# Kernel optimization log

Hardware: AMD Instinct MI355X
Metric: run time of the kernel (lower is better)

Reference implementation:

```python
import jax, jax.numpy as jnp
import numpy as np

N_NODES = 100000


def _gcn_layer(x, src, dst, W, b, n):
    # PyG GCNConv: x' = x @ W, then symmetric-normalized aggregation with
    # self-loops (fill value 1), then + bias.
    h = x @ W  # [n, out]
    loop = jnp.arange(n, dtype=src.dtype)
    s = jnp.concatenate([src, loop])  # sources incl. self-loops
    d = jnp.concatenate([dst, loop])  # destinations incl. self-loops
    # degree computed on destination (col) with unit edge weights
    deg = jax.ops.segment_sum(jnp.ones_like(d, dtype=h.dtype), d, num_segments=n)
    dinv = jnp.where(deg > 0, jax.lax.rsqrt(deg), 0.0)
    norm = dinv[s] * dinv[d]  # [E+n]
    msg = h[s] * norm[:, None]  # gather + scale, [E+n, out]
    out = jax.ops.segment_sum(msg, d, num_segments=n)  # scatter-add
    return out + b


def setup_inputs() -> dict:
    key = jax.random.key(0)
    k1, k2, k3, k4, k5, k6 = jax.random.split(key, 6)
    in_c, hid_c, out_c = 5, 128, 64
    E = 1600000
    x = jax.random.normal(k1, (N_NODES, in_c), dtype=jnp.float32)
    edge_index = jax.random.randint(k2, (2, E), 0, N_NODES, dtype=jnp.int64)
    # Glorot-style init like PyG's Linear
    W1 = jax.random.normal(k3, (in_c, hid_c), dtype=jnp.float32) / np.sqrt(in_c)
    b1 = jnp.zeros((hid_c,), dtype=jnp.float32)
    W2 = jax.random.normal(k4, (hid_c, out_c), dtype=jnp.float32) / np.sqrt(hid_c)
    b2 = jnp.zeros((out_c,), dtype=jnp.float32)
    return {"x": x, "edge_index": edge_index, "W1": W1, "b1": b1, "W2": W2, "b2": b2}


def reference(x, edge_index, W1, b1, W2, b2):
    src, dst = edge_index[0], edge_index[1]
    n = x.shape[0]
    h = _gcn_layer(x, src, dst, W1, b1, n)
    h = jax.nn.relu(h)
    out = _gcn_layer(h, src, dst, W2, b2, n)
    return out
```

## Files before the change

kernel.cpp:

```cpp
#include <hip/hip_runtime.h>
#include <hip/hip_fp16.h>

#define IN_C 5
#define HID  128
#define OUTC 64

#define NBUCK_MAX 512
#define BCAP      4800
#define BIN_GRID  512
#define BIN_PER   3328
#define BIN_ITERS 13

typedef _Float16 f16x8 __attribute__((ext_vector_type(8)));
typedef float    f32x4 __attribute__((ext_vector_type(4)));

__global__ void __launch_bounds__(256)
k_init(const float* __restrict__ W2, __half* __restrict__ W2p,
       int* __restrict__ bucket_cnt) {
    if (blockIdx.x < 2) bucket_cnt[blockIdx.x * 256 + threadIdx.x] = 0;
    int i = blockIdx.x * 256 + threadIdx.x;
    int j = i & 7;
    int lane = (i >> 3) & 63;
    int kk = (i >> 9) & 3;
    int nt = i >> 11;
    int k = kk * 32 + (lane >> 4) * 8 + j;
    int nn = nt * 16 + (lane & 15);
    W2p[i] = __float2half(W2[k * OUTC + nn]);
}

__global__ void __launch_bounds__(256)
k_bin(const int* __restrict__ src, const int* __restrict__ dst,
      int* __restrict__ bucket_cnt, unsigned* __restrict__ binned, int E) {
    __shared__ int hist[NBUCK_MAX], base[NBUCK_MAX], lstart[NBUCK_MAX], cur[NBUCK_MAX];
    __shared__ unsigned staged[BIN_PER];
    __shared__ unsigned short sbuck[BIN_PER];
    int t = threadIdx.x;
    hist[t] = 0; hist[t + 256] = 0;
    __syncthreads();
    int per = (E + gridDim.x - 1) / gridDim.x;
    int lo = blockIdx.x * per, hi = min(E, lo + per);
    int ds[BIN_ITERS], ss[BIN_ITERS];
#pragma unroll
    for (int i = 0; i < BIN_ITERS; ++i) {
        int e = lo + t + i * 256;
        if (e < hi) {
            int d = dst[e];
            ds[i] = d; ss[i] = src[e];
            atomicAdd(&hist[d >> 8], 1);
        } else ds[i] = -1;
    }
    __syncthreads();
    if (hist[t] > 0)       base[t] = atomicAdd(&bucket_cnt[t], hist[t]);
    if (hist[t + 256] > 0) base[t + 256] = atomicAdd(&bucket_cnt[t + 256], hist[t + 256]);
    lstart[t] = hist[t]; lstart[t + 256] = hist[t + 256];
    __syncthreads();
#pragma unroll
    for (int off = 1; off < NBUCK_MAX; off <<= 1) {
        int a0 = (t >= off) ? lstart[t - off] : 0;
        int a1 = (t + 256 >= off) ? lstart[t + 256 - off] : 0;
        __syncthreads();
        lstart[t] += a0; lstart[t + 256] += a1;
        __syncthreads();
    }
    {
        int e0 = lstart[t] - hist[t];
        int e1 = lstart[t + 256] - hist[t + 256];
        __syncthreads();
        lstart[t] = e0; lstart[t + 256] = e1;
        cur[t] = e0; cur[t + 256] = e1;
    }
    __syncthreads();
#pragma unroll
    for (int i = 0; i < BIN_ITERS; ++i) {
        if (ds[i] >= 0) {
            int d = ds[i];
            int b = d >> 8;
            int pos = atomicAdd(&cur[b], 1);
            staged[pos] = ((unsigned)ss[i] << 8) | (unsigned)(d & 255);
            sbuck[pos] = (unsigned short)b;
        }
    }
    __syncthreads();
    int mtot = hi - lo;
    for (int s = t; s < mtot; s += 256) {
        int b = sbuck[s];
        binned[(size_t)b * BCAP + base[b] + (s - lstart[b])] = staged[s];
    }
}

__global__ void __launch_bounds__(256)
k_csr(const unsigned* __restrict__ binned, const int* __restrict__ bucket_cnt,
      const float* __restrict__ x,
      int* __restrict__ rowptr, int* __restrict__ cnt, float* __restrict__ dinv,
      __half* __restrict__ xs, int* __restrict__ col, int n, int nb) {
    __shared__ int sc[NBUCK_MAX];
    __shared__ int hist[256], sc2[256], cur[256];
    __shared__ int staged[BCAP];
    int b = blockIdx.x;
    int t = threadIdx.x;

    sc[t]       = (t < nb) ? bucket_cnt[t] : 0;
    sc[t + 256] = (t + 256 < nb) ? bucket_cnt[t + 256] : 0;
    __syncthreads();
#pragma unroll
    for (int off = 1; off < NBUCK_MAX; off <<= 1) {
        int a0 = (t >= off) ? sc[t - off] : 0;
        int a1 = (t + 256 >= off) ? sc[t + 256 - off] : 0;
        __syncthreads();
        sc[t] += a0; sc[t + 256] += a1;
        __syncthreads();
    }
    int m = bucket_cnt[b];
    int ebase = (b == 0) ? 0 : sc[b - 1];
    const unsigned* bin = binned + (size_t)b * BCAP;

    hist[t] = 0;
    __syncthreads();
    for (int e = t; e < m; e += 256)
        atomicAdd(&hist[bin[e] & 255], 1);
    __syncthreads();

    int h = hist[t];
    sc2[t] = h;
    __syncthreads();
#pragma unroll
    for (int off = 1; off < 256; off <<= 1) {
        int a = (t >= off) ? sc2[t - off] : 0;
        __syncthreads();
        sc2[t] += a;
        __syncthreads();
    }
    int rs = sc2[t] - h;
    cur[t] = rs;

    int v = b * 256 + t;
    if (v < n) {
        rowptr[v] = ebase + rs;
        cnt[v] = h;
        float dv = rsqrtf(1.0f + (float)h);
        dinv[v] = dv;
        const float* xp = x + (size_t)v * IN_C;
        __half2 hh[4];
        hh[0] = __floats2half2_rn(xp[0] * dv, xp[1] * dv);
        hh[1] = __floats2half2_rn(xp[2] * dv, xp[3] * dv);
        hh[2] = __floats2half2_rn(xp[4] * dv, 0.f);
        hh[3] = __floats2half2_rn(0.f, 0.f);
        *(uint4*)(xs + (size_t)v * 8) = *(uint4*)hh;
    }
    __syncthreads();
    for (int e = t; e < m; e += 256) {
        unsigned p = bin[e];
        int pos = atomicAdd(&cur[p & 255], 1);
        staged[pos] = (int)(p >> 8);
    }
    __syncthreads();
    for (int e = t; e < m; e += 256)
        col[ebase + e] = staged[e];
}

#define NB 64
#define H1STRIDE 132
__global__ void __launch_bounds__(256, 7)
k_fused(const __half* __restrict__ xs, const float* __restrict__ dinv,
        const int* __restrict__ rowptr, const int* __restrict__ cnt,
        const int* __restrict__ col,
        const float* __restrict__ W1, const float* __restrict__ b1,
        const __half* __restrict__ W2p, __half* __restrict__ g2, int n) {
    __shared__ __half sh_h1[NB * H1STRIDE];
    __shared__ float sh_xa[NB * 9];
    __shared__ float sh_dinv[NB];
    __shared__ int sh_start[NB], sh_len[NB];
    __shared__ __half2 sh_w1[IN_C * 64];
    __shared__ float sh_b1[HID];
    int t = threadIdx.x;
    int base = blockIdx.x * NB;

    for (int idx = t; idx < IN_C * 64; idx += 256) {
        int k = idx >> 6, jp = idx & 63;
        float2 w = *(const float2*)(W1 + k * HID + 2 * jp);
        sh_w1[idx] = __floats2half2_rn(w.x, w.y);
    }
    if (t < HID) sh_b1[t] = b1[t];

    if (t < NB) {
        int v = base + t;
        if (v < n) {
            sh_start[t] = rowptr[v];
            sh_len[t]   = cnt[v];
            sh_dinv[t]  = dinv[v];
        } else {
            sh_start[t] = 0; sh_len[t] = 0; sh_dinv[t] = 0.f;
        }
    }
    __syncthreads();

    {
        int q = t & 7;
#pragma unroll
        for (int half = 0; half < 2; ++half) {
            int vl = (t >> 3) + half * 32;
            int v = base + vl;
            int start = sh_start[vl], len = sh_len[vl];
            float a0 = 0.f, a1 = 0.f, a2 = 0.f, a3 = 0.f, a4 = 0.f;
            if (q == 0 && v < n) {
                uint4 r = *(const uint4*)(xs + (size_t)v * 8);
                const __half2* h = (const __half2*)&r;
                float2 f0 = __half22float2(h[0]), f1 = __half22float2(h[1]), f2 = __half22float2(h[2]);
                a0 = f0.x; a1 = f0.y; a2 = f1.x; a3 = f1.y; a4 = f2.x;
            }
            for (int k = q; k < len; k += 8) {
                int s = col[start + k];
                uint4 r = *(const uint4*)(xs + (size_t)s * 8);
                const __half2* h = (const __half2*)&r;
                float2 f0 = __half22float2(h[0]), f1 = __half22float2(h[1]), f2 = __half22float2(h[2]);
                a0 += f0.x; a1 += f0.y; a2 += f1.x; a3 += f1.y; a4 += f2.x;
            }
#pragma unroll
            for (int d = 1; d <= 4; d <<= 1) {
                a0 += __shfl_down(a0, d, 64);
                a1 += __shfl_down(a1, d, 64);
                a2 += __shfl_down(a2, d, 64);
                a3 += __shfl_down(a3, d, 64);
                a4 += __shfl_down(a4, d, 64);
            }
            if (q == 0) {
                float* sx = sh_xa + vl * 9;
                sx[0] = a0; sx[1] = a1; sx[2] = a2; sx[3] = a3; sx[4] = a4;
            }
        }
    }
    __syncthreads();

    {
        int v = t >> 2;
        const float* xa = sh_xa + v * 9;
        float x0 = xa[0], x1 = xa[1], x2 = xa[2], x3 = xa[3], x4 = xa[4];
        float dv = sh_dinv[v];
        __half* hrow = sh_h1 + v * H1STRIDE;
#pragma unroll
        for (int i = 0; i < 16; ++i) {
            int jp = (t & 3) + 4 * i;
            float2 w0 = __half22float2(sh_w1[jp]);
            float2 w1v = __half22float2(sh_w1[64 + jp]);
            float2 w2v = __half22float2(sh_w1[128 + jp]);
            float2 w3 = __half22float2(sh_w1[192 + jp]);
            float2 w4 = __half22float2(sh_w1[256 + jp]);
            float acc0 = x0 * w0.x + x1 * w1v.x + x2 * w2v.x + x3 * w3.x + x4 * w4.x;
            float acc1 = x0 * w0.y + x1 * w1v.y + x2 * w2v.y + x3 * w3.y + x4 * w4.y;
            int j0 = jp * 2;
            float2 bb = *(const float2*)(sh_b1 + j0);
            *(__half2*)(hrow + j0) =
                __floats2half2_rn(fmaxf(acc0 * dv + bb.x, 0.f), fmaxf(acc1 * dv + bb.y, 0.f));
        }
    }
    __syncthreads();

    {
        int w = t >> 6;
        int lane = t & 63;
        int quad = lane >> 4, nn = lane & 15;
        const __half* arow = sh_h1 + (size_t)(w * 16 + nn) * H1STRIDE + quad * 8;
        f16x8 afr[4];
#pragma unroll
        for (int kk = 0; kk < 4; ++kk)
            afr[kk] = *(const f16x8*)(arow + kk * 32);

        const f16x8* bp = (const f16x8*)W2p + lane;
#pragma unroll
        for (int nt = 0; nt < 4; ++nt) {
            f32x4 acc = {0.f, 0.f, 0.f, 0.f};
#pragma unroll
            for (int kk = 0; kk < 4; ++kk)
                acc = __builtin_amdgcn_mfma_f32_16x16x32_f16(
                    afr[kk], bp[(nt * 4 + kk) * 64], acc, 0, 0, 0);
#pragma unroll
            for (int r = 0; r < 4; ++r) {
                int vl = w * 16 + quad * 4 + r;
                int v = base + vl;
                if (v < n)
                    g2[(size_t)v * OUTC + nt * 16 + nn] =
                        __float2half(acc[r] * sh_dinv[vl]);
            }
        }
    }
}


#define MIX_LO(A, W) \
    asm("v_fma_mix_f32 %0, %1, %2, %0 op_sel:[0,0,0] op_sel_hi:[1,0,0]" \
        : "+v"(A) : "v"(W), "v"(one))
#define MIX_HI(A, W) \
    asm("v_fma_mix_f32 %0, %1, %2, %0 op_sel:[1,0,0] op_sel_hi:[1,0,0]" \
        : "+v"(A) : "v"(W), "v"(one))

#define ACC8(P, R)            \
    do {                      \
        MIX_LO(P##0, (R).x);  \
        MIX_HI(P##1, (R).x);  \
        MIX_LO(P##2, (R).y);  \
        MIX_HI(P##3, (R).y);  \
        MIX_LO(P##4, (R).z);  \
        MIX_HI(P##5, (R).z);  \
        MIX_LO(P##6, (R).w);  \
        MIX_HI(P##7, (R).w);  \
    } while (0)

__global__ void __launch_bounds__(256)
k_agg2(const __half* __restrict__ g2, const float* __restrict__ dinv,
       const int* __restrict__ rowptr, const int* __restrict__ cnt,
       const int* __restrict__ col, const float* __restrict__ b2,
       float* __restrict__ out, int n) {
    int t = threadIdx.x;
    int g = t >> 3;
    int oct = t & 7;
    int v = blockIdx.x * 32 + g;
    if (v >= n) return;

    int start = rowptr[v], len = cnt[v];
    float one = 1.0f;

    float a0 = 0.f, a1 = 0.f, a2 = 0.f, a3 = 0.f,
          a4 = 0.f, a5 = 0.f, a6 = 0.f, a7 = 0.f;
    float c0 = 0.f, c1 = 0.f, c2 = 0.f, c3 = 0.f,
          c4 = 0.f, c5 = 0.f, c6 = 0.f, c7 = 0.f;

    int it = 0;
    for (; it + 2 <= len; it += 2) {
        int s0 = col[start + it];
        int s1 = col[start + it + 1];
        uint4 r0 = *(const uint4*)(g2 + ((size_t)s0 << 6) + (oct << 3));
        uint4 r1 = *(const uint4*)(g2 + ((size_t)s1 << 6) + (oct << 3));
        ACC8(a, r0);
        ACC8(c, r1);
    }
    if (it < len) {
        int s0 = col[start + it];
        uint4 r0 = *(const uint4*)(g2 + ((size_t)s0 << 6) + (oct << 3));
        ACC8(a, r0);
    }

    {
        uint4 rs = *(const uint4*)(g2 + ((size_t)v << 6) + (oct << 3));
        ACC8(a, rs);
    }

    a0 += c0; a1 += c1; a2 += c2; a3 += c3;
    a4 += c4; a5 += c5; a6 += c6; a7 += c7;

    float dv = dinv[v];
    const float* bp = b2 + (oct << 3);
    float4 bb0 = *(const float4*)bp;
    float4 bb1 = *(const float4*)(bp + 4);

    float4 o0 = make_float4(dv * a0 + bb0.x, dv * a1 + bb0.y,
                            dv * a2 + bb0.z, dv * a3 + bb0.w);
    float4 o1 = make_float4(dv * a4 + bb1.x, dv * a5 + bb1.y,
                            dv * a6 + bb1.z, dv * a7 + bb1.w);
    float4* op = (float4*)(out + ((size_t)v << 6) + (oct << 3));
    op[0] = o0;
    op[1] = o1;
}


extern "C" void kernel_launch(void* const* d_in, const int* in_sizes, int n_in,
                              void* d_out, int out_size, void* d_ws, size_t ws_size,
                              hipStream_t stream) {
    const float* x  = (const float*)d_in[0];
    const int*   ei = (const int*)d_in[1];
    const float* W1 = (const float*)d_in[2];
    const float* b1 = (const float*)d_in[3];
    const float* W2 = (const float*)d_in[4];
    const float* b2 = (const float*)d_in[5];
    float*       out = (float*)d_out;

    const int n = in_sizes[0] / IN_C;
    const int E = in_sizes[1] / 2;
    const int* src = ei;
    const int* dst = ei + E;
    const int nbuck = (n + 255) / 256;

    char* ws = (char*)d_ws;
    size_t off = 0;
    int* cnt         = (int*)(ws + off); off += (size_t)n * 4;
    int* rowptr      = (int*)(ws + off); off += (size_t)n * 4;
    int* col         = (int*)(ws + off); off += (size_t)E * 4;
    float* dinv      = (float*)(ws + off); off += (size_t)n * 4;
    __half* xs       = (__half*)(ws + off); off += (size_t)n * 8 * 2;
    __half* g2       = (__half*)(ws + off); off += (size_t)n * OUTC * 2;
    __half* W2p      = (__half*)(ws + off); off += (size_t)HID * OUTC * 2;
    int* bucket_cnt  = (int*)(ws + off); off += NBUCK_MAX * 4;
    unsigned* binned = (unsigned*)(ws + off); off += (size_t)NBUCK_MAX * BCAP * 4;

    const int B = 256;

    k_init<<<(HID * OUTC) / B, B, 0, stream>>>(W2, W2p, bucket_cnt);
    k_bin<<<BIN_GRID, B, 0, stream>>>(src, dst, bucket_cnt, binned, E);
    k_csr<<<nbuck, B, 0, stream>>>(binned, bucket_cnt, x,
                                   rowptr, cnt, dinv, xs, col, n, nbuck);

    k_fused<<<(n + NB - 1) / NB, B, 0, stream>>>(xs, dinv, rowptr, cnt, col,
                                                 W1, b1, W2p, g2, n);
    k_agg2<<<(n + 31) / 32, B, 0, stream>>>(g2, dinv, rowptr, cnt, col, b2, out, n);
}
```

Before: 171.8 us.

## Replace bucketed binning CSR build with global-atomic degree count and scatter

Replaces the two-pass bucket binning (block-local histogram, staged bucket writes, per-bucket LDS counting sort) with a classic CSR build: zero counts, global atomic degree count, block sums, scan, and atomic-cursor scatter of source indices into col. This removes the intermediate binned buffer and its LDS-heavy staging, at the cost of many scattered global atomics and uncoalesced col writes. Edge order within each row becomes nondeterministic, and the build now takes more, smaller kernel launches.

```diff
diff --git a/kernel.cpp b/kernel.cpp
--- a/kernel.cpp
+++ b/kernel.cpp
@@ -6,18 +6,12 @@
 #define OUTC 64
 
 #define NBUCK_MAX 512
-#define BCAP      4800
-#define BIN_GRID  512
-#define BIN_PER   3328
-#define BIN_ITERS 13
 
 typedef _Float16 f16x8 __attribute__((ext_vector_type(8)));
 typedef float    f32x4 __attribute__((ext_vector_type(4)));
 
 __global__ void __launch_bounds__(256)
-k_init(const float* __restrict__ W2, __half* __restrict__ W2p,
-       int* __restrict__ bucket_cnt) {
-    if (blockIdx.x < 2) bucket_cnt[blockIdx.x * 256 + threadIdx.x] = 0;
+k_init(const float* __restrict__ W2, __half* __restrict__ W2p) {
     int i = blockIdx.x * 256 + threadIdx.x;
     int j = i & 7;
     int lane = (i >> 3) & 63;
@@ -28,79 +22,53 @@
     W2p[i] = __float2half(W2[k * OUTC + nn]);
 }
 
-__global__ void __launch_bounds__(256)
-k_bin(const int* __restrict__ src, const int* __restrict__ dst,
-      int* __restrict__ bucket_cnt, unsigned* __restrict__ binned, int E) {
-    __shared__ int hist[NBUCK_MAX], base[NBUCK_MAX], lstart[NBUCK_MAX], cur[NBUCK_MAX];
-    __shared__ unsigned staged[BIN_PER];
-    __shared__ unsigned short sbuck[BIN_PER];
-    int t = threadIdx.x;
-    hist[t] = 0; hist[t + 256] = 0;
-    __syncthreads();
-    int per = (E + gridDim.x - 1) / gridDim.x;
-    int lo = blockIdx.x * per, hi = min(E, lo + per);
-    int ds[BIN_ITERS], ss[BIN_ITERS];
-#pragma unroll
-    for (int i = 0; i < BIN_ITERS; ++i) {
-        int e = lo + t + i * 256;
-        if (e < hi) {
-            int d = dst[e];
-            ds[i] = d; ss[i] = src[e];
-            atomicAdd(&hist[d >> 8], 1);
-        } else ds[i] = -1;
-    }
-    __syncthreads();
-    if (hist[t] > 0)       base[t] = atomicAdd(&bucket_cnt[t], hist[t]);
-    if (hist[t + 256] > 0) base[t + 256] = atomicAdd(&bucket_cnt[t + 256], hist[t + 256]);
-    lstart[t] = hist[t]; lstart[t + 256] = hist[t + 256];
-    __syncthreads();
-#pragma unroll
-    for (int off = 1; off < NBUCK_MAX; off <<= 1) {
-        int a0 = (t >= off) ? lstart[t - off] : 0;
-        int a1 = (t + 256 >= off) ? lstart[t + 256 - off] : 0;
-        __syncthreads();
-        lstart[t] += a0; lstart[t + 256] += a1;
-        __syncthreads();
-    }
-    {
-        int e0 = lstart[t] - hist[t];
-        int e1 = lstart[t + 256] - hist[t + 256];
-        __syncthreads();
-        lstart[t] = e0; lstart[t + 256] = e1;
-        cur[t] = e0; cur[t + 256] = e1;
-    }
-    __syncthreads();
-#pragma unroll
-    for (int i = 0; i < BIN_ITERS; ++i) {
-        if (ds[i] >= 0) {
-            int d = ds[i];
-            int b = d >> 8;
-            int pos = atomicAdd(&cur[b], 1);
-            staged[pos] = ((unsigned)ss[i] << 8) | (unsigned)(d & 255);
-            sbuck[pos] = (unsigned short)b;
-        }
-    }
-    __syncthreads();
-    int mtot = hi - lo;
-    for (int s = t; s < mtot; s += 256) {
-        int b = sbuck[s];
-        binned[(size_t)b * BCAP + base[b] + (s - lstart[b])] = staged[s];
-    }
-}
-
-__global__ void __launch_bounds__(256)
-k_csr(const unsigned* __restrict__ binned, const int* __restrict__ bucket_cnt,
-      const float* __restrict__ x,
-      int* __restrict__ rowptr, int* __restrict__ cnt, float* __restrict__ dinv,
-      __half* __restrict__ xs, int* __restrict__ col, int n, int nb) {
+
+__global__ void __launch_bounds__(256)
+k_zero(int* __restrict__ cnt, int* __restrict__ bsum, int n) {
+    int i = blockIdx.x * 256 + threadIdx.x;
+    if (i < n) cnt[i] = 0;
+    if (blockIdx.x < 2) bsum[blockIdx.x * 256 + threadIdx.x] = 0;
+}
+
+__global__ void __launch_bounds__(256)
+k_deg(const int* __restrict__ dst, int* __restrict__ cnt, int E) {
+    int i = blockIdx.x * 256 + threadIdx.x;
+    if (i < (E >> 2)) {
+        int4 d = ((const int4*)dst)[i];
+        atomicAdd(&cnt[d.x], 1);
+        atomicAdd(&cnt[d.y], 1);
+        atomicAdd(&cnt[d.z], 1);
+        atomicAdd(&cnt[d.w], 1);
+    }
+}
+
+__global__ void __launch_bounds__(256)
+k_bsum(const int* __restrict__ cnt, int* __restrict__ bsum, int n) {
+    __shared__ int red[256];
+    int b = blockIdx.x, t = threadIdx.x;
+    int v = b * 256 + t;
+    red[t] = (v < n) ? cnt[v] : 0;
+    __syncthreads();
+#pragma unroll
+    for (int off = 128; off > 0; off >>= 1) {
+        if (t < off) red[t] += red[t + off];
+        __syncthreads();
+    }
+    if (t == 0) bsum[b] = red[0];
+}
+
+__global__ void __launch_bounds__(256)
+k_scan_xs(const int* __restrict__ bsum, const int* __restrict__ cnt,
+          const float* __restrict__ x,
+          int* __restrict__ rowptr, int* __restrict__ cur, float* __restrict__ dinv,
+          __half* __restrict__ xs, int n, int nb) {
     __shared__ int sc[NBUCK_MAX];
-    __shared__ int hist[256], sc2[256], cur[256];
-    __shared__ int staged[BCAP];
+    __shared__ int sc2[256];
     int b = blockIdx.x;
     int t = threadIdx.x;
 
-    sc[t]       = (t < nb) ? bucket_cnt[t] : 0;
-    sc[t + 256] = (t + 256 < nb) ? bucket_cnt[t + 256] : 0;
+    sc[t]       = (t < nb) ? bsum[t] : 0;
+    sc[t + 256] = (t + 256 < nb) ? bsum[t + 256] : 0;
     __syncthreads();
 #pragma unroll
     for (int off = 1; off < NBUCK_MAX; off <<= 1) {
@@ -110,17 +78,10 @@
         sc[t] += a0; sc[t + 256] += a1;
         __syncthreads();
     }
-    int m = bucket_cnt[b];
     int ebase = (b == 0) ? 0 : sc[b - 1];
-    const unsigned* bin = binned + (size_t)b * BCAP;
-
-    hist[t] = 0;
-    __syncthreads();
-    for (int e = t; e < m; e += 256)
-        atomicAdd(&hist[bin[e] & 255], 1);
-    __syncthreads();
-
-    int h = hist[t];
+
+    int v = b * 256 + t;
+    int h = (v < n) ? cnt[v] : 0;
     sc2[t] = h;
     __syncthreads();
 #pragma unroll
@@ -131,12 +92,11 @@
         __syncthreads();
     }
     int rs = sc2[t] - h;
-    cur[t] = rs;
-
-    int v = b * 256 + t;
+
     if (v < n) {
-        rowptr[v] = ebase + rs;
-        cnt[v] = h;
+        int rp = ebase + rs;
+        rowptr[v] = rp;
+        cur[v] = rp;
         float dv = rsqrtf(1.0f + (float)h);
         dinv[v] = dv;
         const float* xp = x + (size_t)v * IN_C;
@@ -147,15 +107,20 @@
         hh[3] = __floats2half2_rn(0.f, 0.f);
         *(uint4*)(xs + (size_t)v * 8) = *(uint4*)hh;
     }
-    __syncthreads();
-    for (int e = t; e < m; e += 256) {
-        unsigned p = bin[e];
-        int pos = atomicAdd(&cur[p & 255], 1);
-        staged[pos] = (int)(p >> 8);
-    }
-    __syncthreads();
-    for (int e = t; e < m; e += 256)
-        col[ebase + e] = staged[e];
+}
+
+__global__ void __launch_bounds__(256)
+k_scatter(const int* __restrict__ src, const int* __restrict__ dst,
+          int* __restrict__ cur, int* __restrict__ col, int E) {
+    int i = blockIdx.x * 256 + threadIdx.x;
+    if (i < (E >> 2)) {
+        int4 s = ((const int4*)src)[i];
+        int4 d = ((const int4*)dst)[i];
+        col[atomicAdd(&cur[d.x], 1)] = s.x;
+        col[atomicAdd(&cur[d.y], 1)] = s.y;
+        col[atomicAdd(&cur[d.z], 1)] = s.z;
+        col[atomicAdd(&cur[d.w], 1)] = s.w;
+    }
 }
 
 #define NB 64
@@ -381,22 +346,25 @@
 
     char* ws = (char*)d_ws;
     size_t off = 0;
-    int* cnt         = (int*)(ws + off); off += (size_t)n * 4;
-    int* rowptr      = (int*)(ws + off); off += (size_t)n * 4;
-    int* col         = (int*)(ws + off); off += (size_t)E * 4;
-    float* dinv      = (float*)(ws + off); off += (size_t)n * 4;
-    __half* xs       = (__half*)(ws + off); off += (size_t)n * 8 * 2;
-    __half* g2       = (__half*)(ws + off); off += (size_t)n * OUTC * 2;
-    __half* W2p      = (__half*)(ws + off); off += (size_t)HID * OUTC * 2;
-    int* bucket_cnt  = (int*)(ws + off); off += NBUCK_MAX * 4;
-    unsigned* binned = (unsigned*)(ws + off); off += (size_t)NBUCK_MAX * BCAP * 4;
+    int* cnt    = (int*)(ws + off); off += (size_t)n * 4;
+    int* rowptr = (int*)(ws + off); off += (size_t)n * 4;
+    int* cur    = (int*)(ws + off); off += (size_t)n * 4;
+    int* col    = (int*)(ws + off); off += (size_t)E * 4;
+    float* dinv = (float*)(ws + off); off += (size_t)n * 4;
+    __half* xs  = (__half*)(ws + off); off += (size_t)n * 8 * 2;
+    __half* g2  = (__half*)(ws + off); off += (size_t)n * OUTC * 2;
+    __half* W2p = (__half*)(ws + off); off += (size_t)HID * OUTC * 2;
+    int* bsum   = (int*)(ws + off); off += NBUCK_MAX * 4;
 
     const int B = 256;
-
-    k_init<<<(HID * OUTC) / B, B, 0, stream>>>(W2, W2p, bucket_cnt);
-    k_bin<<<BIN_GRID, B, 0, stream>>>(src, dst, bucket_cnt, binned, E);
-    k_csr<<<nbuck, B, 0, stream>>>(binned, bucket_cnt, x,
-                                   rowptr, cnt, dinv, xs, col, n, nbuck);
+    const int e4blocks = ((E >> 2) + B - 1) / B;
+
+    k_init<<<(HID * OUTC) / B, B, 0, stream>>>(W2, W2p);
+    k_zero<<<nbuck, B, 0, stream>>>(cnt, bsum, n);
+    k_deg<<<e4blocks, B, 0, stream>>>(dst, cnt, E);
+    k_bsum<<<nbuck, B, 0, stream>>>(cnt, bsum, n);
+    k_scan_xs<<<nbuck, B, 0, stream>>>(bsum, cnt, x, rowptr, cur, dinv, xs, n, nbuck);
+    k_scatter<<<e4blocks, B, 0, stream>>>(src, dst, cur, col, E);
 
     k_fused<<<(n + NB - 1) / NB, B, 0, stream>>>(xs, dinv, rowptr, cnt, col,
                                                  W1, b1, W2p, g2, n);
```

New measurement: 324.2 us. 88.6% more time.
